# Optimization experiments

Hardware: AMD Instinct MI355X
Metric: run time of the kernel (lower is better)

The kernel has to match this reference:

```python
import jax, jax.numpy as jnp
import numpy as np

# --- SLAYER hyperparameters (from netParams) ---
THETA = 10.0        # spike threshold
TAU_SR = 10.0       # SRM alpha-kernel time constant (ms)
TAU_RHO = 1.0       # surrogate-gradient width
SCALE_RHO = 1.0     # surrogate-gradient scale
TS = 1.0            # simulation step (ms)
T_SAMPLE = 300      # number of time steps
K_LEN = 64          # truncated SRM kernel length

N_BATCH, N_IN, N_HID, N_OUT = 128, 784, 410, 10


def srm_kernel():
    # SRM-alpha kernel eps(t) = (t/tau) * exp(1 - t/tau), sampled at Ts, eps(0)=0
    t = jnp.arange(K_LEN, dtype=jnp.float32) * TS
    return (t / TAU_SR) * jnp.exp(1.0 - t / TAU_SR)


def psp(x):
    # Causal FIR filtering along time: out[t] = sum_k eps[k] * x[t-k]
    # x: [N, C, T]
    n, c, t = x.shape
    kern = srm_kernel()
    lhs = x.reshape(n * c, 1, t)
    rhs = kern[::-1].reshape(1, 1, K_LEN)  # flip: conv_general_dilated is cross-correlation
    out = jax.lax.conv_general_dilated(
        lhs, rhs, window_strides=(1,), padding=[(K_LEN - 1, 0)],
        dimension_numbers=("NCH", "OIH", "NCH"))
    return out.reshape(n, c, t)


@jax.custom_vjp
def spike_fn(u):
    # Heaviside threshold with surrogate gradient rho(u) = (scale/tau) * exp(-|u-theta|/tau)
    return (u >= THETA).astype(u.dtype)

def _spike_fwd(u):
    return spike_fn(u), u

def _spike_bwd(u, g):
    return (g * (SCALE_RHO / TAU_RHO) * jnp.exp(-jnp.abs(u - THETA) / TAU_RHO),)

spike_fn.defvjp(_spike_fwd, _spike_bwd)


def setup_inputs() -> dict:
    key = jax.random.key(0)
    k1, k2, k3, k4 = jax.random.split(key, 4)
    img = jax.random.uniform(k1, (N_BATCH, N_IN), dtype=jnp.float32)
    rand_u = jax.random.uniform(k2, (N_BATCH, N_IN, T_SAMPLE), dtype=jnp.float32)
    W1 = jax.random.normal(k3, (N_HID, N_IN), dtype=jnp.float32)
    W2 = jax.random.normal(k4, (N_OUT, N_HID), dtype=jnp.float32)
    return {"img": img, "rand_u": rand_u, "W1": W1, "W2": W2}


def reference(img, rand_u, W1, W2):
    # Poisson spike encoding: spike whenever uniform noise < pixel intensity
    s0 = (rand_u < img[:, :, None]).astype(jnp.float32)        # [N, 784, T]
    # fc1 (dense over spatial features, shared over time) -> psp -> spike
    a1 = jnp.einsum("nit,oi->not", s0, W1)                     # [N, 410, T]
    s1 = spike_fn(psp(a1))
    # fc2 -> psp -> spike
    a2 = jnp.einsum("nht,oh->not", s1, W2)                     # [N, 10, T]
    s2 = spike_fn(psp(a2))
    return s2
```

## Files before the change

### kernel.cpp

```cpp
#include <hip/hip_runtime.h>
#include <cstdint>
#include <cstddef>

#define N_B 128
#define N_I 784
#define N_H 410
#define N_O 10
#define TT  300
#define KL  64
#define NW  26
#define NKS 13
#define NTILES 26
#define NHP 416
#define SSTR 448
#define NKS2 7
#define NDIG 4
#define ASTRIDE 848

typedef int v4i __attribute__((ext_vector_type(4)));

__device__ __forceinline__ uint32_t expand4(uint32_t v) {
  return (v * 0x00204081u) & 0x01010101u;
}

__global__ void k_pack(const float* __restrict__ rand_u, const float* __restrict__ img,
                       uint32_t* __restrict__ s0w) {
  int n = blockIdx.y;
  int t = blockIdx.x * 64 + threadIdx.x;
  if (t >= TT) return;
  const float* rb = rand_u + (size_t)n * N_I * TT + t;
  const float* ib = img + (size_t)n * N_I;
  uint32_t* dst = s0w + ((size_t)n * TT + t) * NW;
  #pragma unroll 1
  for (int w = 0; w < 25; ++w) {
    int ib32 = w * 32;
    float r[32];
    #pragma unroll
    for (int b = 0; b < 32; ++b) {
      int i = ib32 + b;
      r[b] = (i < N_I) ? rb[(size_t)i * TT] : 2.0f;
    }
    uint32_t bits = 0;
    #pragma unroll
    for (int b = 0; b < 32; ++b) {
      int i = ib32 + b;
      float p = (i < N_I) ? ib[i] : 0.0f;
      bits |= (r[b] < p ? 1u : 0u) << b;
    }
    dst[w] = bits;
  }
  dst[25] = 0;
}

__global__ void k_eps(double* __restrict__ epsb) {
  int k = threadIdx.x;
  if (k < KL) {
    double td = (double)k;
    double e = (td / 10.0) * exp(1.0 - td / 10.0);
    epsb[k] = e;
    epsb[KL + k] = e * (1.0 / 268435456.0);
  }
}

__global__ void k_bprep(const float* __restrict__ W1, v4i* __restrict__ Bf) {
  int bid  = blockIdx.x;
  int lane = threadIdx.x;
  int ks   = bid % NKS;
  int rest = bid / NKS;
  int nt   = rest % NTILES;
  int d    = rest / NTILES;
  int o     = nt * 16 + (lane & 15);
  int kbase = ks * 64 + (lane >> 4) * 16;
  uint32_t wds[4] = {0, 0, 0, 0};
  for (int j = 0; j < 16; ++j) {
    int k = kbase + j;
    int dig = 0;
    if (o < N_H && k < N_I) {
      double w = (double)W1[(size_t)o * N_I + k];
      int r = (int)llround(w * 268435456.0);
      for (int dd = 0; dd <= d; ++dd) {
        dig = (int)(int8_t)(uint8_t)(r & 255);
        r = (r - dig) >> 8;
      }
    }
    wds[j >> 2] |= ((uint32_t)(uint8_t)(int8_t)dig) << (8 * (j & 3));
  }
  v4i v; v[0] = (int)wds[0]; v[1] = (int)wds[1]; v[2] = (int)wds[2]; v[3] = (int)wds[3];
  Bf[(size_t)bid * 64 + lane] = v;
}

__global__ void k_bprep2(const float* __restrict__ W2, v4i* __restrict__ Bf2) {
  int bid  = blockIdx.x;
  int lane = threadIdx.x;
  int ks = bid % NKS2, d = bid / NKS2;
  int o     = lane & 15;
  int kbase = ks * 64 + (lane >> 4) * 16;
  uint32_t wds[4] = {0, 0, 0, 0};
  for (int j = 0; j < 16; ++j) {
    int k = kbase + j;
    int dig = 0;
    if (o < N_O && k < N_H) {
      double w = (double)W2[(size_t)o * N_H + k];
      int r = (int)llround(w * 268435456.0);
      for (int dd = 0; dd <= d; ++dd) {
        dig = (int)(int8_t)(uint8_t)(r & 255);
        r = (r - dig) >> 8;
      }
    }
    wds[j >> 2] |= ((uint32_t)(uint8_t)(int8_t)dig) << (8 * (j & 3));
  }
  v4i v; v[0] = (int)wds[0]; v[1] = (int)wds[1]; v[2] = (int)wds[2]; v[3] = (int)wds[3];
  Bf2[(size_t)bid * 64 + lane] = v;
}

__global__ __launch_bounds__(256, 2) void k_gemm1m(const uint32_t* __restrict__ s0w,
                                                   const v4i* __restrict__ Bf,
                                                   double* __restrict__ a1, int rowbase) {
  __shared__ __attribute__((aligned(16))) uint8_t Alds[64 * ASTRIDE];
  int tid = threadIdx.x;
  int mb = blockIdx.x, nb = blockIdx.y;
  const uint32_t* wbase = s0w + (size_t)(rowbase + mb * 64) * NW;
  for (int idx = tid; idx < 64 * NW; idx += 256) {
    int row = idx / NW;
    int w = idx - row * NW;
    uint32_t bits = wbase[idx];
    uint4 q0, q1;
    q0.x = expand4(bits & 0xF);         q0.y = expand4((bits >> 4) & 0xF);
    q0.z = expand4((bits >> 8) & 0xF);  q0.w = expand4((bits >> 12) & 0xF);
    q1.x = expand4((bits >> 16) & 0xF); q1.y = expand4((bits >> 20) & 0xF);
    q1.z = expand4((bits >> 24) & 0xF); q1.w = expand4((bits >> 28) & 0xF);
    uint8_t* dst = &Alds[(size_t)row * ASTRIDE + w * 32];
    *(uint4*)dst = q0;
    *(uint4*)(dst + 16) = q1;
  }
  __syncthreads();
  int wave = tid >> 6, lane = tid & 63;
  int nt = nb * 4 + wave;
  if (nt >= NTILES) return;
  int lrow = lane & 15, quad = lane >> 4;
  const v4i* bb = Bf + (size_t)nt * NKS * 64 + lane;
  const size_t dstr = (size_t)NTILES * NKS * 64;
  v4i acc[4][NDIG];
  #pragma unroll
  for (int mt = 0; mt < 4; ++mt)
    #pragma unroll
    for (int d = 0; d < NDIG; ++d) { acc[mt][d][0]=0; acc[mt][d][1]=0; acc[mt][d][2]=0; acc[mt][d][3]=0; }
  uint32_t abase[4];
  #pragma unroll
  for (int mt = 0; mt < 4; ++mt) abase[mt] = (uint32_t)((mt * 16 + lrow) * ASTRIDE + quad * 16);
  for (int ks = 0; ks < NKS; ++ks) {
    v4i af[4];
    #pragma unroll
    for (int mt = 0; mt < 4; ++mt) af[mt] = *(const v4i*)&Alds[abase[mt] + ks * 64];
    v4i bf[NDIG];
    #pragma unroll
    for (int d = 0; d < NDIG; ++d) bf[d] = bb[(size_t)d * dstr + ks * 64];
    #pragma unroll
    for (int mt = 0; mt < 4; ++mt)
      #pragma unroll
      for (int d = 0; d < NDIG; ++d)
        acc[mt][d] = __builtin_amdgcn_mfma_i32_16x16x64_i8(af[mt], bf[d], acc[mt][d], 0, 0, 0);
  }
  int o = nt * 16 + lrow;
  #pragma unroll
  for (int mt = 0; mt < 4; ++mt)
    #pragma unroll
    for (int r = 0; r < 4; ++r) {
      int m = mb * 64 + mt * 16 + quad * 4 + r;
      double v = (double)acc[mt][0][r]
               + 256.0      * (double)acc[mt][1][r]
               + 65536.0    * (double)acc[mt][2][r]
               + 16777216.0 * (double)acc[mt][3][r];
      a1[(size_t)m * NHP + o] = v;
    }
}

__global__ __launch_bounds__(128) void k_fir1i(const double* __restrict__ a1,
                                               uint8_t* __restrict__ s1) {
  __shared__ double ring[64][104];
  int col = threadIdx.x;
  if (col >= 104) return;
  int o   = blockIdx.x * 104 + col;
  int seg = blockIdx.y;
  int nn  = blockIdx.z;
  const double q   = exp(-0.1);
  const double q64 = exp(-6.4);
  const double cS  = (exp(1.0) / 10.0) * (1.0 / 268435456.0);
  int T0 = seg * 150, T1 = T0 + 150;
  int W = T0 - 63; if (W < 0) W = 0;
  const double* base = a1 + (size_t)nn * TT * NHP + o;
  uint8_t* sbase = s1 + (size_t)nn * TT * SSTR + o;
  double s1a = 0.0, s2a = 0.0, s1b = 0.0, s2b = 0.0;
  #pragma unroll 4
  for (int p = W; p < T0; ++p) {
    double x = base[(size_t)p * NHP];
    ring[p & 63][col] = x;
    s2a = q * (s2a + s1a);
    s1a = q * s1a + x;
  }
  int tB = W + 64; if (tB > T1) tB = T1;
  #pragma unroll 4
  for (int t = T0; t < tB; ++t) {
    double x = base[(size_t)t * NHP];
    ring[t & 63][col] = x;
    s2a = q * (s2a + s1a);
    s1a = q * s1a + x;
    sbase[(size_t)t * SSTR] = (cS * s2a >= 10.0) ? 1 : 0;
  }
  #pragma unroll 4
  for (int t = tB; t < T1; ++t) {
    double xb = ring[t & 63][col];
    double xa = base[(size_t)t * NHP];
    ring[t & 63][col] = xa;
    s2b = q * (s2b + s1b);
    s1b = q * s1b + xb;
    s2a = q * (s2a + s1a);
    s1a = q * s1a + xa;
    double y = cS * (s2a - q64 * (s2b + 64.0 * s1b));
    sbase[(size_t)t * SSTR] = (y >= 10.0) ? 1 : 0;
  }
}

__global__ void k_gemm2m(const uint8_t* __restrict__ s1, const v4i* __restrict__ Bf2,
                         double* __restrict__ a2) {
  int tid = threadIdx.x;
  int wave = tid >> 6, lane = tid & 63;
  int m0 = (blockIdx.x * 4 + wave) * 16;
  int lrow = lane & 15, quad = lane >> 4;
  v4i acc[NDIG];
  #pragma unroll
  for (int d = 0; d < NDIG; ++d) { acc[d][0]=0; acc[d][1]=0; acc[d][2]=0; acc[d][3]=0; }
  const uint8_t* arow = s1 + (size_t)(m0 + lrow) * SSTR + quad * 16;
  for (int ks = 0; ks < NKS2; ++ks) {
    v4i af = *(const v4i*)(arow + ks * 64);
    #pragma unroll
    for (int d = 0; d < NDIG; ++d) {
      v4i bf = Bf2[(size_t)(d * NKS2 + ks) * 64 + lane];
      acc[d] = __builtin_amdgcn_mfma_i32_16x16x64_i8(af, bf, acc[d], 0, 0, 0);
    }
  }
  int o = lrow;
  if (o < N_O) {
    #pragma unroll
    for (int r = 0; r < 4; ++r) {
      int m = m0 + quad * 4 + r;
      int nn = m / TT;
      int t = m - nn * TT;
      double v = (double)acc[0][r]
               + 256.0      * (double)acc[1][r]
               + 65536.0    * (double)acc[2][r]
               + 16777216.0 * (double)acc[3][r];
      a2[((size_t)nn * N_O + o) * TT + t] = v;
    }
  }
}

__global__ void k_fir2(const double* __restrict__ a2, const double* __restrict__ epsb,
                       float* __restrict__ out, int n0, int nc) {
  int flat = blockIdx.x * 256 + threadIdx.x;
  if (flat >= nc * N_O * TT) return;
  int t    = flat % TT;
  int rest = flat / TT;
  int o    = rest % N_O;
  int nn   = rest / N_O;
  const double* arow = a2 + ((size_t)nn * N_O + o) * TT;
  const double* epsS = epsb + KL;
  double u = 0.0;
  int kmax = (t < KL - 1) ? t : (KL - 1);
  for (int k = 0; k <= kmax; ++k) u += epsS[k] * arow[t - k];
  out[(((size_t)(n0 + nn)) * N_O + o) * TT + t] = (u >= 10.0) ? 1.0f : 0.0f;
}

extern "C" void kernel_launch(void* const* d_in, const int* in_sizes, int n_in,
                              void* d_out, int out_size, void* d_ws, size_t ws_size,
                              hipStream_t stream) {
  const float* img   = (const float*)d_in[0];
  const float* randu = (const float*)d_in[1];
  const float* W1    = (const float*)d_in[2];
  const float* W2    = (const float*)d_in[3];
  float* out = (float*)d_out;

  const size_t fixedB = (((size_t)N_B * TT * NW * 4 + 511) & ~511UL)
                      + (((size_t)NDIG * NTILES * NKS * 64 * 16 + 511) & ~511UL)
                      + (((size_t)NDIG * NKS2 * 64 * 16 + 511) & ~511UL)
                      + ((128 * 8 + 511) & ~511UL);
  const size_t perN = (size_t)TT * NHP * 8 + (size_t)TT * SSTR + (size_t)N_O * TT * 8;
  int nc = 16;
  const int cands[3] = {128, 64, 32};
  for (int ci = 0; ci < 3; ++ci)
    if (fixedB + (size_t)cands[ci] * perN + 8192 <= ws_size) { nc = cands[ci]; break; }
  const int nchunk = N_B / nc;

  char* ws = (char*)d_ws;
  size_t off = 0;
  auto alloc = [&](size_t bytes) -> void* {
    void* p = ws + off;
    off = (off + bytes + 511) & ~(size_t)511;
    return p;
  };
  uint32_t* s0w  = (uint32_t*)alloc((size_t)N_B * TT * NW * sizeof(uint32_t));
  v4i*      Bf   = (v4i*)     alloc((size_t)NDIG * NTILES * NKS * 64 * 16);
  v4i*      Bf2  = (v4i*)     alloc((size_t)NDIG * NKS2 * 64 * 16);
  double*   epsb = (double*)  alloc(128 * sizeof(double));
  double*   a1   = (double*)  alloc((size_t)nc * TT * NHP * sizeof(double));
  uint8_t*  s1   = (uint8_t*) alloc((size_t)nc * TT * SSTR);
  double*   a2   = (double*)  alloc((size_t)nc * N_O * TT * sizeof(double));
  if (off > ws_size) return;

  k_pack  <<<dim3(5, N_B), 64, 0, stream>>>(randu, img, s0w);
  k_eps   <<<dim3(1), 64, 0, stream>>>(epsb);
  k_bprep <<<dim3(NDIG * NTILES * NKS), 64, 0, stream>>>(W1, Bf);
  k_bprep2<<<dim3(NDIG * NKS2), 64, 0, stream>>>(W2, Bf2);

  for (int c = 0; c < nchunk; ++c) {
    int n0 = c * nc;
    k_gemm1m<<<dim3(nc * TT / 64, 7),             256, 0, stream>>>(s0w, Bf, a1, n0 * TT);
    k_fir1i <<<dim3(4, 2, nc),                    128, 0, stream>>>(a1, s1);
    k_gemm2m<<<dim3(nc * TT / 64),                256, 0, stream>>>(s1, Bf2, a2);
    k_fir2  <<<dim3((nc * N_O * TT + 255) / 256), 256, 0, stream>>>(a2, epsb, out, n0, nc);
  }
}
```

Before: 358.9 us.

## Fuse layer-1 GEMM with PSP filter and spike, dropping a1 buffer

Replaces the separate layer-1 int8 MFMA GEMM and FIR/spike kernels with one kernel per (hidden tile, batch). It walks time in 64-step chunks, keeps the double-precision GEMM results in a double-buffered shared tile and runs the recursive alpha-filter in-block, so the large a1 buffer never goes to global memory. A operands are expanded from packed bits straight into registers with software prefetch instead of staged through LDS. The batch chunking loop is removed. In exchange each block is a single wave and only 16 lanes run the serial filter, which may limit parallelism and occupancy.

```diff
diff --git a/kernel.cpp b/kernel.cpp
--- a/kernel.cpp
+++ b/kernel.cpp
@@ -11,11 +11,9 @@
 #define NW  26
 #define NKS 13
 #define NTILES 26
-#define NHP 416
 #define SSTR 448
 #define NKS2 7
 #define NDIG 4
-#define ASTRIDE 848
 
 typedef int v4i __attribute__((ext_vector_type(4)));
 
@@ -113,111 +111,107 @@
   Bf2[(size_t)bid * 64 + lane] = v;
 }
 
-__global__ __launch_bounds__(256, 2) void k_gemm1m(const uint32_t* __restrict__ s0w,
-                                                   const v4i* __restrict__ Bf,
-                                                   double* __restrict__ a1, int rowbase) {
-  __shared__ __attribute__((aligned(16))) uint8_t Alds[64 * ASTRIDE];
-  int tid = threadIdx.x;
-  int mb = blockIdx.x, nb = blockIdx.y;
-  const uint32_t* wbase = s0w + (size_t)(rowbase + mb * 64) * NW;
-  for (int idx = tid; idx < 64 * NW; idx += 256) {
-    int row = idx / NW;
-    int w = idx - row * NW;
-    uint32_t bits = wbase[idx];
-    uint4 q0, q1;
-    q0.x = expand4(bits & 0xF);         q0.y = expand4((bits >> 4) & 0xF);
-    q0.z = expand4((bits >> 8) & 0xF);  q0.w = expand4((bits >> 12) & 0xF);
-    q1.x = expand4((bits >> 16) & 0xF); q1.y = expand4((bits >> 20) & 0xF);
-    q1.z = expand4((bits >> 24) & 0xF); q1.w = expand4((bits >> 28) & 0xF);
-    uint8_t* dst = &Alds[(size_t)row * ASTRIDE + w * 32];
-    *(uint4*)dst = q0;
-    *(uint4*)(dst + 16) = q1;
-  }
-  __syncthreads();
-  int wave = tid >> 6, lane = tid & 63;
-  int nt = nb * 4 + wave;
-  if (nt >= NTILES) return;
+__global__ __launch_bounds__(64) void k_fused(const uint32_t* __restrict__ s0w,
+                                              const v4i* __restrict__ Bf,
+                                              uint8_t* __restrict__ s1) {
+  __shared__ double tile[2][64][17];
+  __shared__ __attribute__((aligned(16))) uint8_t btile[64][16];
+  int lane = threadIdx.x;
+  int nt = blockIdx.x, n = blockIdx.y;
   int lrow = lane & 15, quad = lane >> 4;
-  const v4i* bb = Bf + (size_t)nt * NKS * 64 + lane;
-  const size_t dstr = (size_t)NTILES * NKS * 64;
-  v4i acc[4][NDIG];
-  #pragma unroll
-  for (int mt = 0; mt < 4; ++mt)
-    #pragma unroll
-    for (int d = 0; d < NDIG; ++d) { acc[mt][d][0]=0; acc[mt][d][1]=0; acc[mt][d][2]=0; acc[mt][d][3]=0; }
-  uint32_t abase[4];
-  #pragma unroll
-  for (int mt = 0; mt < 4; ++mt) abase[mt] = (uint32_t)((mt * 16 + lrow) * ASTRIDE + quad * 16);
-  for (int ks = 0; ks < NKS; ++ks) {
-    v4i af[4];
-    #pragma unroll
-    for (int mt = 0; mt < 4; ++mt) af[mt] = *(const v4i*)&Alds[abase[mt] + ks * 64];
-    v4i bf[NDIG];
-    #pragma unroll
-    for (int d = 0; d < NDIG; ++d) bf[d] = bb[(size_t)d * dstr + ks * 64];
-    #pragma unroll
-    for (int mt = 0; mt < 4; ++mt)
-      #pragma unroll
-      for (int d = 0; d < NDIG; ++d)
-        acc[mt][d] = __builtin_amdgcn_mfma_i32_16x16x64_i8(af[mt], bf[d], acc[mt][d], 0, 0, 0);
-  }
-  int o = nt * 16 + lrow;
-  #pragma unroll
-  for (int mt = 0; mt < 4; ++mt)
-    #pragma unroll
-    for (int r = 0; r < 4; ++r) {
-      int m = mb * 64 + mt * 16 + quad * 4 + r;
-      double v = (double)acc[mt][0][r]
-               + 256.0      * (double)acc[mt][1][r]
-               + 65536.0    * (double)acc[mt][2][r]
-               + 16777216.0 * (double)acc[mt][3][r];
-      a1[(size_t)m * NHP + o] = v;
-    }
-}
-
-__global__ __launch_bounds__(128) void k_fir1i(const double* __restrict__ a1,
-                                               uint8_t* __restrict__ s1) {
-  __shared__ double ring[64][104];
-  int col = threadIdx.x;
-  if (col >= 104) return;
-  int o   = blockIdx.x * 104 + col;
-  int seg = blockIdx.y;
-  int nn  = blockIdx.z;
+  int wsel = quad >> 1, hsel = (quad & 1) * 16;
   const double q   = exp(-0.1);
   const double q64 = exp(-6.4);
   const double cS  = (exp(1.0) / 10.0) * (1.0 / 268435456.0);
-  int T0 = seg * 150, T1 = T0 + 150;
-  int W = T0 - 63; if (W < 0) W = 0;
-  const double* base = a1 + (size_t)nn * TT * NHP + o;
-  uint8_t* sbase = s1 + (size_t)nn * TT * SSTR + o;
   double s1a = 0.0, s2a = 0.0, s1b = 0.0, s2b = 0.0;
-  #pragma unroll 4
-  for (int p = W; p < T0; ++p) {
-    double x = base[(size_t)p * NHP];
-    ring[p & 63][col] = x;
-    s2a = q * (s2a + s1a);
-    s1a = q * s1a + x;
-  }
-  int tB = W + 64; if (tB > T1) tB = T1;
-  #pragma unroll 4
-  for (int t = T0; t < tB; ++t) {
-    double x = base[(size_t)t * NHP];
-    ring[t & 63][col] = x;
-    s2a = q * (s2a + s1a);
-    s1a = q * s1a + x;
-    sbase[(size_t)t * SSTR] = (cS * s2a >= 10.0) ? 1 : 0;
-  }
-  #pragma unroll 4
-  for (int t = tB; t < T1; ++t) {
-    double xb = ring[t & 63][col];
-    double xa = base[(size_t)t * NHP];
-    ring[t & 63][col] = xa;
-    s2b = q * (s2b + s1b);
-    s1b = q * s1b + xb;
-    s2a = q * (s2a + s1a);
-    s1a = q * s1a + xa;
-    double y = cS * (s2a - q64 * (s2b + 64.0 * s1b));
-    sbase[(size_t)t * SSTR] = (y >= 10.0) ? 1 : 0;
+  const v4i* bb = Bf + (size_t)nt * NKS * 64 + lane;
+  const size_t dstr = (size_t)NTILES * NKS * 64;
+  const uint32_t* srow = s0w + (size_t)n * TT * NW;
+  uint8_t* sbase = s1 + (size_t)n * TT * SSTR + nt * 16;
+
+  for (int ch = 0; ch < 5; ++ch) {
+    int t0 = ch * 64;
+    v4i acc[4][NDIG];
+    #pragma unroll
+    for (int mt = 0; mt < 4; ++mt)
+      #pragma unroll
+      for (int d = 0; d < NDIG; ++d) { acc[mt][d][0]=0; acc[mt][d][1]=0; acc[mt][d][2]=0; acc[mt][d][3]=0; }
+
+    v4i bcur[NDIG]; uint32_t acur[4];
+    #pragma unroll
+    for (int d = 0; d < NDIG; ++d) bcur[d] = bb[(size_t)d * dstr];
+    #pragma unroll
+    for (int mt = 0; mt < 4; ++mt) {
+      int row = t0 + mt * 16 + lrow; if (row > TT - 1) row = TT - 1;
+      acur[mt] = srow[(size_t)row * NW + wsel];
+    }
+    for (int ks = 0; ks < NKS; ++ks) {
+      int ks2 = (ks + 1 < NKS) ? ks + 1 : ks;
+      v4i bnxt[NDIG]; uint32_t anxt[4];
+      #pragma unroll
+      for (int d = 0; d < NDIG; ++d) bnxt[d] = bb[(size_t)d * dstr + ks2 * 64];
+      #pragma unroll
+      for (int mt = 0; mt < 4; ++mt) {
+        int row = t0 + mt * 16 + lrow; if (row > TT - 1) row = TT - 1;
+        anxt[mt] = srow[(size_t)row * NW + ks2 * 2 + wsel];
+      }
+      #pragma unroll
+      for (int mt = 0; mt < 4; ++mt) {
+        uint32_t h = (acur[mt] >> hsel) & 0xFFFFu;
+        v4i af;
+        af[0] = (int)expand4(h & 0xF);
+        af[1] = (int)expand4((h >> 4) & 0xF);
+        af[2] = (int)expand4((h >> 8) & 0xF);
+        af[3] = (int)expand4((h >> 12) & 0xF);
+        #pragma unroll
+        for (int d = 0; d < NDIG; ++d)
+          acc[mt][d] = __builtin_amdgcn_mfma_i32_16x16x64_i8(af, bcur[d], acc[mt][d], 0, 0, 0);
+      }
+      #pragma unroll
+      for (int d = 0; d < NDIG; ++d) bcur[d] = bnxt[d];
+      #pragma unroll
+      for (int mt = 0; mt < 4; ++mt) acur[mt] = anxt[mt];
+    }
+
+    int tb = ch & 1;
+    #pragma unroll
+    for (int mt = 0; mt < 4; ++mt)
+      #pragma unroll
+      for (int r = 0; r < 4; ++r) {
+        double v = (double)acc[mt][0][r]
+                 + 256.0      * (double)acc[mt][1][r]
+                 + 65536.0    * (double)acc[mt][2][r]
+                 + 16777216.0 * (double)acc[mt][3][r];
+        tile[tb][mt * 16 + quad * 4 + r][lrow] = v;
+      }
+
+    int jmax = TT - t0; if (jmax > 64) jmax = 64;
+    if (lane < 16) {
+      if (ch == 0) {
+        for (int j = 0; j < jmax; ++j) {
+          double xa = tile[0][j][lane];
+          s2a = q * (s2a + s1a);
+          s1a = q * s1a + xa;
+          btile[j][lane] = (cS * s2a >= 10.0) ? 1 : 0;
+        }
+      } else {
+        for (int j = 0; j < jmax; ++j) {
+          double xb = tile[tb ^ 1][j][lane];
+          double xa = tile[tb][j][lane];
+          s2b = q * (s2b + s1b);
+          s1b = q * s1b + xb;
+          s2a = q * (s2a + s1a);
+          s1a = q * s1a + xa;
+          double y = cS * (s2a - q64 * (s2b + 64.0 * s1b));
+          btile[j][lane] = (y >= 10.0) ? 1 : 0;
+        }
+      }
+    }
+
+    if (lane < jmax) {
+      uint4 v = *(const uint4*)&btile[lane][0];
+      *(uint4*)(sbase + (size_t)(t0 + lane) * SSTR) = v;
+    }
   }
 }
 
@@ -256,9 +250,9 @@
 }
 
 __global__ void k_fir2(const double* __restrict__ a2, const double* __restrict__ epsb,
-                       float* __restrict__ out, int n0, int nc) {
+                       float* __restrict__ out) {
   int flat = blockIdx.x * 256 + threadIdx.x;
-  if (flat >= nc * N_O * TT) return;
+  if (flat >= N_B * N_O * TT) return;
   int t    = flat % TT;
   int rest = flat / TT;
   int o    = rest % N_O;
@@ -268,7 +262,7 @@
   double u = 0.0;
   int kmax = (t < KL - 1) ? t : (KL - 1);
   for (int k = 0; k <= kmax; ++k) u += epsS[k] * arow[t - k];
-  out[(((size_t)(n0 + nn)) * N_O + o) * TT + t] = (u >= 10.0) ? 1.0f : 0.0f;
+  out[((size_t)nn * N_O + o) * TT + t] = (u >= 10.0) ? 1.0f : 0.0f;
 }
 
 extern "C" void kernel_launch(void* const* d_in, const int* in_sizes, int n_in,
@@ -279,17 +273,6 @@
   const float* W1    = (const float*)d_in[2];
   const float* W2    = (const float*)d_in[3];
   float* out = (float*)d_out;
-
-  const size_t fixedB = (((size_t)N_B * TT * NW * 4 + 511) & ~511UL)
-                      + (((size_t)NDIG * NTILES * NKS * 64 * 16 + 511) & ~511UL)
-                      + (((size_t)NDIG * NKS2 * 64 * 16 + 511) & ~511UL)
-                      + ((128 * 8 + 511) & ~511UL);
-  const size_t perN = (size_t)TT * NHP * 8 + (size_t)TT * SSTR + (size_t)N_O * TT * 8;
-  int nc = 16;
-  const int cands[3] = {128, 64, 32};
-  for (int ci = 0; ci < 3; ++ci)
-    if (fixedB + (size_t)cands[ci] * perN + 8192 <= ws_size) { nc = cands[ci]; break; }
-  const int nchunk = N_B / nc;
 
   char* ws = (char*)d_ws;
   size_t off = 0;
@@ -302,9 +285,8 @@
   v4i*      Bf   = (v4i*)     alloc((size_t)NDIG * NTILES * NKS * 64 * 16);
   v4i*      Bf2  = (v4i*)     alloc((size_t)NDIG * NKS2 * 64 * 16);
   double*   epsb = (double*)  alloc(128 * sizeof(double));
-  double*   a1   = (double*)  alloc((size_t)nc * TT * NHP * sizeof(double));
-  uint8_t*  s1   = (uint8_t*) alloc((size_t)nc * TT * SSTR);
-  double*   a2   = (double*)  alloc((size_t)nc * N_O * TT * sizeof(double));
+  uint8_t*  s1   = (uint8_t*) alloc((size_t)N_B * TT * SSTR);
+  double*   a2   = (double*)  alloc((size_t)N_B * N_O * TT * sizeof(double));
   if (off > ws_size) return;
 
   k_pack  <<<dim3(5, N_B), 64, 0, stream>>>(randu, img, s0w);
@@ -312,11 +294,7 @@
   k_bprep <<<dim3(NDIG * NTILES * NKS), 64, 0, stream>>>(W1, Bf);
   k_bprep2<<<dim3(NDIG * NKS2), 64, 0, stream>>>(W2, Bf2);
 
-  for (int c = 0; c < nchunk; ++c) {
-    int n0 = c * nc;
-    k_gemm1m<<<dim3(nc * TT / 64, 7),             256, 0, stream>>>(s0w, Bf, a1, n0 * TT);
-    k_fir1i <<<dim3(4, 2, nc),                    128, 0, stream>>>(a1, s1);
-    k_gemm2m<<<dim3(nc * TT / 64),                256, 0, stream>>>(s1, Bf2, a2);
-    k_fir2  <<<dim3((nc * N_O * TT + 255) / 256), 256, 0, stream>>>(a2, epsb, out, n0, nc);
-  }
-}
+  k_fused <<<dim3(NTILES, N_B), 64, 0, stream>>>(s0w, Bf, s1);
+  k_gemm2m<<<dim3(N_B * TT / 64), 256, 0, stream>>>(s1, Bf2, a2);
+  k_fir2  <<<dim3((N_B * N_O * TT + 255) / 256), 256, 0, stream>>>(a2, epsb, out);
+}
```

New measurement: 363.7 us. About the same (+1.3%).
